# Kernel tuning notes

Measured on AMD Instinct MI355X. Metric: run time of the kernel, lower is better.

Reference implementation:

```python
import jax, jax.numpy as jnp
import numpy as np

B, Q, H, HKV, D = 4, 1024, 32, 8, 128
HID = H * D            # 4096
BS = 16                # block_size
BLOCKS_PER_SEQ = Q // BS  # 64
NB = B * BLOCKS_PER_SEQ   # 256 total cache blocks
THETA = 10000.0
SCALE = D ** -0.5


def _rope(x, pos):
    # x: [T, h, D] (NeoX half-split rotary), pos: [T] int
    inv = 1.0 / (THETA ** (jnp.arange(0, D, 2, dtype=jnp.float32) / D))  # [D/2]
    ang = pos[:, None].astype(jnp.float32) * inv                          # [T, D/2]
    cos = jnp.cos(ang)[:, None, :]
    sin = jnp.sin(ang)[:, None, :]
    x1, x2 = jnp.split(x, 2, axis=-1)
    return jnp.concatenate([x1 * cos - x2 * sin, x1 * sin + x2 * cos], axis=-1).astype(x.dtype)


def setup_inputs() -> dict:
    key = jax.random.key(0)
    ks = jax.random.split(key, 3)
    hidden_states = jax.random.normal(ks[0], (B * Q, HID), dtype=jnp.float32)
    w_qkv = jax.random.normal(ks[1], (HID, (H + 2 * HKV) * D), dtype=jnp.float32) * 0.02
    w_o = jax.random.normal(ks[2], (H * D, HID), dtype=jnp.float32) * 0.02
    key_cache = jnp.zeros((NB, BS, HKV, D), dtype=jnp.float32)
    value_cache = jnp.zeros((NB, BS, HKV, D), dtype=jnp.float32)
    positions = jnp.tile(jnp.arange(Q, dtype=jnp.int32), B)          # context_len=0 prefill
    slot_mapping = jnp.arange(B * Q, dtype=jnp.int32)                # contiguous slots
    block_tables = jnp.arange(NB, dtype=jnp.int32).reshape(B, BLOCKS_PER_SEQ)
    return {"hidden_states": hidden_states, "w_qkv": w_qkv, "w_o": w_o,
            "key_cache": key_cache, "value_cache": value_cache,
            "positions": positions, "slot_mapping": slot_mapping,
            "block_tables": block_tables}


def reference(hidden_states, w_qkv, w_o, key_cache, value_cache, positions, slot_mapping, block_tables):
    # QKV projection and split (q_size = H*D, kv_size = HKV*D)
    qkv = hidden_states @ w_qkv
    q, k, v = jnp.split(qkv, [H * D, H * D + HKV * D], axis=-1)
    q = q.reshape(-1, H, D)
    k = k.reshape(-1, HKV, D)
    v = v.reshape(-1, HKV, D)
    q = _rope(q, positions)
    k = _rope(k, positions)
    # BlockedKVCache.write: slot -> (slot // BS, slot % BS); flatten block dims
    kc = key_cache.reshape(NB * BS, HKV, D).at[slot_mapping].set(k)
    vc = value_cache.reshape(NB * BS, HKV, D).at[slot_mapping].set(v)
    # BlockedKVCache.gather via block_table: [B, blocks, BS, HKV, D] -> [B, S, HKV, D]
    gk = kc.reshape(NB, BS, HKV, D)[block_tables].reshape(B, Q, HKV, D)
    gv = vc.reshape(NB, BS, HKV, D)[block_tables].reshape(B, Q, HKV, D)
    # repeat_kv (GQA): each kv head repeated consecutively
    rep = H // HKV
    gk = jnp.repeat(gk, rep, axis=2)   # [B, S, H, D]
    gv = jnp.repeat(gv, rep, axis=2)
    qb = q.reshape(B, Q, H, D)
    scores = jnp.einsum('bqhd,bshd->bhqs', qb, gk) * SCALE
    # visible = context_len + token_idx + 1 with context_len=0 -> causal mask
    causal = jnp.arange(Q)[None, :] <= jnp.arange(Q)[:, None]          # [q, s]
    scores = jnp.where(causal[None, None], scores.astype(jnp.float32), -jnp.inf)
    probs = jax.nn.softmax(scores, axis=-1).astype(qb.dtype)
    attn = jnp.einsum('bhqs,bshd->bqhd', probs, gv).reshape(B * Q, H * D)
    return attn @ w_o
```

## Files before the change

### kernel.cpp

```cpp
#include <hip/hip_runtime.h>
#include <stdint.h>

typedef short short8  __attribute__((ext_vector_type(8)));
typedef short short4v __attribute__((ext_vector_type(4)));
typedef float f32x4   __attribute__((ext_vector_type(4)));

#define B_    4
#define Q_    1024
#define H_    32
#define HKV_  8
#define D_    128
#define HID_  4096
#define NQKV_ 6144
#define SCALE_ 0.08838834764831845f

__device__ __forceinline__ short f2bf(float f) {
  unsigned u = __builtin_bit_cast(unsigned, f);
  u += 0x7fffu + ((u >> 16) & 1u);
  return (short)(u >> 16);
}
__device__ __forceinline__ float bf2f(short s) {
  unsigned u = ((unsigned)(unsigned short)s) << 16;
  return __builtin_bit_cast(float, u);
}

__device__ __forceinline__ void gload_lds16(const void* g, void* l) {
  __builtin_amdgcn_global_load_lds(
      (__attribute__((address_space(1))) void*)(uintptr_t)(g),
      (__attribute__((address_space(3))) void*)(l), 16, 0, 0);
}

__device__ __forceinline__ f32x4 mfma16x16x32(short8 a, short8 b, f32x4 c) {
  return __builtin_amdgcn_mfma_f32_16x16x32_bf16(a, b, c, 0, 0, 0);
}

__global__ __launch_bounds__(256) void k_cvt(const float* __restrict__ src,
                                             short* __restrict__ dst, int n) {
  int i = (blockIdx.x * 256 + threadIdx.x) * 4;
  if (i + 3 < n) {
    float4 v = *reinterpret_cast<const float4*>(src + i);
    short4v o;
    o[0] = f2bf(v.x); o[1] = f2bf(v.y); o[2] = f2bf(v.z); o[3] = f2bf(v.w);
    *reinterpret_cast<short4v*>(dst + i) = o;
  }
}

__global__ __launch_bounds__(256) void k_cvt_t(const float* __restrict__ src,
                                               short* __restrict__ dst, int R, int C) {
  __shared__ float tile[32][33];
  int c0 = blockIdx.x * 32, r0 = blockIdx.y * 32;
  int tx = threadIdx.x & 31, ty = threadIdx.x >> 5;
#pragma unroll
  for (int i = 0; i < 4; ++i)
    tile[ty + i * 8][tx] = src[(size_t)(r0 + ty + i * 8) * C + c0 + tx];
  __syncthreads();
#pragma unroll
  for (int i = 0; i < 4; ++i)
    dst[(size_t)(c0 + ty + i * 8) * R + r0 + tx] = f2bf(tile[tx][ty + i * 8]);
}

__global__ __launch_bounds__(256) void k_gemm1(const short* __restrict__ A,
                                               const short* __restrict__ Bt,
                                               short* __restrict__ qout,
                                               short* __restrict__ kvout) {
  __shared__ alignas(16) short Asm[128 * 32];
  __shared__ alignas(16) short Bsm[128 * 32];
  const int tid = threadIdx.x;
  const int wave = tid >> 6, lane = tid & 63;
  const int G = lane >> 4, r = lane & 15;
  const int wm = wave >> 1, wn = wave & 1;
  const size_t Arow0 = (size_t)blockIdx.y * 128;
  const size_t Brow0 = (size_t)blockIdx.x * 128;
  const int K = HID_;
  const int ldrow = lane >> 2, ldcol = (lane & 3) * 8;
  short* Cb; size_t ldc, cb;
  if (Brow0 < (size_t)HID_) { Cb = qout; ldc = HID_; cb = Brow0; }
  else                      { Cb = kvout; ldc = 2048; cb = Brow0 - HID_; }
  f32x4 acc[4][4] = {};
  for (int k0 = 0; k0 < K; k0 += 32) {
    __syncthreads();
#pragma unroll
    for (int i = 0; i < 2; ++i) {
      int c = wave * 2 + i;
      gload_lds16(A + (Arow0 + c * 16 + ldrow) * K + k0 + ldcol, &Asm[c * 512]);
      gload_lds16(Bt + (Brow0 + c * 16 + ldrow) * K + k0 + ldcol, &Bsm[c * 512]);
    }
    asm volatile("s_waitcnt vmcnt(0)" ::: "memory");
    __syncthreads();
    short8 af[4], bf[4];
#pragma unroll
    for (int i = 0; i < 4; ++i)
      af[i] = *reinterpret_cast<const short8*>(&Asm[(wm * 64 + i * 16 + r) * 32 + G * 8]);
#pragma unroll
    for (int j = 0; j < 4; ++j)
      bf[j] = *reinterpret_cast<const short8*>(&Bsm[(wn * 64 + j * 16 + r) * 32 + G * 8]);
#pragma unroll
    for (int i = 0; i < 4; ++i)
#pragma unroll
      for (int j = 0; j < 4; ++j)
        acc[i][j] = mfma16x16x32(af[i], bf[j], acc[i][j]);
  }
#pragma unroll
  for (int i = 0; i < 4; ++i)
#pragma unroll
    for (int j = 0; j < 4; ++j)
#pragma unroll
      for (int rr = 0; rr < 4; ++rr) {
        size_t row = Arow0 + wm * 64 + i * 16 + G * 4 + rr;
        size_t col = cb + wn * 64 + j * 16 + r;
        Cb[row * ldc + col] = f2bf(acc[i][j][rr]);
      }
}

__global__ __launch_bounds__(256) void k_gemm2(const short* __restrict__ A,
                                               const short* __restrict__ Bt,
                                               float* __restrict__ C) {
  __shared__ alignas(16) short Asm[128 * 32];
  __shared__ alignas(16) short Bsm[128 * 32];
  const int tid = threadIdx.x;
  const int wave = tid >> 6, lane = tid & 63;
  const int G = lane >> 4, r = lane & 15;
  const int wm = wave >> 1, wn = wave & 1;
  const size_t Arow0 = (size_t)blockIdx.y * 128;
  const size_t Brow0 = (size_t)blockIdx.x * 128;
  const int K = HID_;
  const int ldrow = lane >> 2, ldcol = (lane & 3) * 8;
  f32x4 acc[4][4] = {};
  for (int k0 = 0; k0 < K; k0 += 32) {
    __syncthreads();
#pragma unroll
    for (int i = 0; i < 2; ++i) {
      int c = wave * 2 + i;
      gload_lds16(A + (Arow0 + c * 16 + ldrow) * K + k0 + ldcol, &Asm[c * 512]);
      gload_lds16(Bt + (Brow0 + c * 16 + ldrow) * K + k0 + ldcol, &Bsm[c * 512]);
    }
    asm volatile("s_waitcnt vmcnt(0)" ::: "memory");
    __syncthreads();
    short8 af[4], bf[4];
#pragma unroll
    for (int i = 0; i < 4; ++i)
      af[i] = *reinterpret_cast<const short8*>(&Asm[(wm * 64 + i * 16 + r) * 32 + G * 8]);
#pragma unroll
    for (int j = 0; j < 4; ++j)
      bf[j] = *reinterpret_cast<const short8*>(&Bsm[(wn * 64 + j * 16 + r) * 32 + G * 8]);
#pragma unroll
    for (int i = 0; i < 4; ++i)
#pragma unroll
      for (int j = 0; j < 4; ++j)
        acc[i][j] = mfma16x16x32(af[i], bf[j], acc[i][j]);
  }
#pragma unroll
  for (int i = 0; i < 4; ++i)
#pragma unroll
    for (int j = 0; j < 4; ++j)
#pragma unroll
      for (int rr = 0; rr < 4; ++rr) {
        size_t row = Arow0 + wm * 64 + i * 16 + G * 4 + rr;
        size_t col = Brow0 + wn * 64 + j * 16 + r;
        C[row * (size_t)HID_ + col] = acc[i][j][rr];
      }
}

__global__ __launch_bounds__(256) void k_rope_bf(short* __restrict__ x, int nh, int ld) {
  const int t = blockIdx.x;
  const float pos = (float)(t & (Q_ - 1));
  short* row = x + (size_t)t * ld;
  for (int i = threadIdx.x; i < nh * 64; i += 256) {
    int h = i >> 6, j = i & 63;
    float fr = powf(10000.0f, -(float)j * (1.0f / 64.0f));
    float sn, cs;
    sincosf(pos * fr, &sn, &cs);
    float x1 = bf2f(row[h * D_ + j]);
    float x2 = bf2f(row[h * D_ + 64 + j]);
    row[h * D_ + j]      = f2bf(x1 * cs - x2 * sn);
    row[h * D_ + 64 + j] = f2bf(x1 * sn + x2 * cs);
  }
}

__global__ __launch_bounds__(256) void k_attn(const short* __restrict__ qbf,
                                              const short* __restrict__ kv,
                                              short* __restrict__ attn) {
  const int qt = blockIdx.x;
  const int h  = blockIdx.y;
  const int b  = blockIdx.z;
  const int hkv = h >> 2;
  const int tid = threadIdx.x, wave = tid >> 6, lane = tid & 63;
  const int G = lane >> 4, r = lane & 15;
  const int q0w = qt * 64 + wave * 16;
  const float NEG_INF = -__builtin_inff();
  __shared__ alignas(16) short Ksm[32 * 136];
  __shared__ alignas(16) short Vsm[128 * 40];
  __shared__ alignas(16) short Psm[4][16][40];
  short8 qf[4];
  {
    const short* qrow = qbf + ((size_t)(b * Q_ + q0w + r)) * HID_ + h * D_;
#pragma unroll
    for (int ds = 0; ds < 4; ++ds)
      qf[ds] = *reinterpret_cast<const short8*>(qrow + ds * 32 + G * 8);
    const float pos = (float)(q0w + r);
#pragma unroll
    for (int ds2 = 0; ds2 < 2; ++ds2)
#pragma unroll
      for (int u = 0; u < 8; ++u) {
        int d = ds2 * 32 + G * 8 + u;
        float fr = powf(10000.0f, -(float)d * (1.0f / 64.0f));
        float sn, cs;
        sincosf(pos * fr, &sn, &cs);
        float x1 = bf2f(qf[ds2][u]);
        float x2 = bf2f(qf[ds2 + 2][u]);
        qf[ds2][u]     = f2bf(x1 * cs - x2 * sn);
        qf[ds2 + 2][u] = f2bf(x1 * sn + x2 * cs);
      }
  }
  f32x4 acc[8] = {};
  float m_run = NEG_INF, l_run = 0.f;
  const int ntiles = qt * 2 + 2;
  const int my_q = q0w + r;
  const int my_q_hi = q0w + 15;
  const int krow = tid >> 3, kd0 = (tid & 7) * 16;
  const int vs = tid & 31, vdg = tid >> 5;
  for (int st = 0; st < ntiles; ++st) {
    __syncthreads();
    {
      const short* gk = kv + ((size_t)(b * Q_ + st * 32 + krow)) * 2048 + hkv * D_ + kd0;
      *reinterpret_cast<uint4*>(&Ksm[krow * 136 + kd0])     = *reinterpret_cast<const uint4*>(gk);
      *reinterpret_cast<uint4*>(&Ksm[krow * 136 + kd0 + 8]) = *reinterpret_cast<const uint4*>(gk + 8);
      const short* gv = kv + ((size_t)(b * Q_ + st * 32 + vs)) * 2048 + 1024 + hkv * D_ + vdg * 16;
      short tmp[16];
      *reinterpret_cast<uint4*>(&tmp[0]) = *reinterpret_cast<const uint4*>(gv);
      *reinterpret_cast<uint4*>(&tmp[8]) = *reinterpret_cast<const uint4*>(gv + 8);
#pragma unroll
      for (int i = 0; i < 16; ++i) Vsm[(vdg * 16 + i) * 40 + vs] = tmp[i];
    }
    __syncthreads();
    if (st * 32 <= my_q_hi) {
      f32x4 sacc[2] = {};
#pragma unroll
      for (int sb = 0; sb < 2; ++sb)
#pragma unroll
        for (int ds = 0; ds < 4; ++ds) {
          short8 kf = *reinterpret_cast<const short8*>(&Ksm[(sb * 16 + r) * 136 + ds * 32 + G * 8]);
          sacc[sb] = mfma16x16x32(kf, qf[ds], sacc[sb]);
        }
      float vals[8];
      float mymax = NEG_INF;
#pragma unroll
      for (int sb = 0; sb < 2; ++sb)
#pragma unroll
        for (int j = 0; j < 4; ++j) {
          int sIdx = st * 32 + sb * 16 + G * 4 + j;
          float v = sacc[sb][j] * SCALE_;
          v = (sIdx <= my_q) ? v : NEG_INF;
          vals[sb * 4 + j] = v;
          mymax = fmaxf(mymax, v);
        }
      mymax = fmaxf(mymax, __shfl_xor(mymax, 16));
      mymax = fmaxf(mymax, __shfl_xor(mymax, 32));
      float m_new = fmaxf(m_run, mymax);
      float factor = __expf(m_run - m_new);
      float psum = 0.f;
      float pv_[8];
#pragma unroll
      for (int i = 0; i < 8; ++i) {
        float p = __expf(vals[i] - m_new);
        psum += p;
        pv_[i] = p;
      }
      psum += __shfl_xor(psum, 16);
      psum += __shfl_xor(psum, 32);
      l_run = l_run * factor + psum;
      m_run = m_new;
#pragma unroll
      for (int i = 0; i < 8; ++i)
        Psm[wave][r][(i >> 2) * 16 + G * 4 + (i & 3)] = f2bf(pv_[i]);
      asm volatile("s_waitcnt lgkmcnt(0)" ::: "memory");
      __builtin_amdgcn_sched_barrier(0);
      short8 pf = *reinterpret_cast<const short8*>(&Psm[wave][r][G * 8]);
      float frow[4];
#pragma unroll
      for (int rr = 0; rr < 4; ++rr) frow[rr] = __shfl(factor, G * 4 + rr);
#pragma unroll
      for (int dt = 0; dt < 8; ++dt)
#pragma unroll
        for (int rr = 0; rr < 4; ++rr) acc[dt][rr] *= frow[rr];
#pragma unroll
      for (int dt = 0; dt < 8; ++dt) {
        short8 vf = *reinterpret_cast<const short8*>(&Vsm[(dt * 16 + r) * 40 + G * 8]);
        acc[dt] = mfma16x16x32(pf, vf, acc[dt]);
      }
    }
  }
  float inv = 1.0f / l_run;
  float irow[4];
#pragma unroll
  for (int rr = 0; rr < 4; ++rr) irow[rr] = __shfl(inv, G * 4 + rr);
#pragma unroll
  for (int dt = 0; dt < 8; ++dt)
#pragma unroll
    for (int rr = 0; rr < 4; ++rr) {
      size_t rowi = (size_t)(b * Q_ + q0w + G * 4 + rr) * HID_;
      attn[rowi + h * D_ + dt * 16 + r] = f2bf(acc[dt][rr] * irow[rr]);
    }
}

extern "C" void kernel_launch(void* const* d_in, const int* in_sizes, int n_in,
                              void* d_out, int out_size, void* d_ws, size_t ws_size,
                              hipStream_t stream) {
  const float* hidden = (const float*)d_in[0];
  const float* w_qkv  = (const float*)d_in[1];
  const float* w_o    = (const float*)d_in[2];
  float* out = (float*)d_out;
  char* ws = (char*)d_ws;
  char* od = (char*)d_out;
  short* hid_bf  = (short*)(od + 0);
  short* q_bf    = (short*)(od + 33554432);
  short* wqkvT   = (short*)(ws + 0);
  short* kv_ws   = (short*)(ws + 50331648);
  short* attn_bf = (short*)(ws + 0);
  short* woT     = (short*)(ws + 33554432);

  k_cvt<<<dim3(16384), dim3(256), 0, stream>>>(hidden, hid_bf, HID_ * B_ * Q_);
  k_cvt_t<<<dim3(192, 128), dim3(256), 0, stream>>>(w_qkv, wqkvT, HID_, NQKV_);
  k_gemm1<<<dim3(48, 32), dim3(256), 0, stream>>>(hid_bf, wqkvT, q_bf, kv_ws);
  k_rope_bf<<<dim3(B_ * Q_), dim3(256), 0, stream>>>(kv_ws, HKV_, 2048);
  k_attn<<<dim3(16, 32, 4), dim3(256), 0, stream>>>(q_bf, kv_ws, attn_bf);
  k_cvt_t<<<dim3(128, 128), dim3(256), 0, stream>>>(w_o, woT, HID_, HID_);
  k_gemm2<<<dim3(32, 32), dim3(256), 0, stream>>>(attn_bf, woT, out);
}
```

Baseline: 684.1 us.

## Replace GEMM kernels with 4-stage pipelined 512-thread templated GEMM

Merges the two bf16 GEMM kernels into one templated kernel with a 4-deep LDS ring buffer. It issues global-to-LDS loads three k-tiles ahead and uses partial vmcnt waits in place of a full drain each iteration. Tiles grow to 128x256 for the QKV projection and 256x256 for the output projection, using 8 waves per block and raising MFMA priority during compute. This targets exposed memory latency and per-tile sync overhead, at the cost of more LDS and registers, which may reduce occupancy, and fewer blocks in the grid.

```diff
diff --git a/kernel.cpp b/kernel.cpp
--- a/kernel.cpp
+++ b/kernel.cpp
@@ -34,6 +34,14 @@
   return __builtin_amdgcn_mfma_f32_16x16x32_bf16(a, b, c, 0, 0, 0);
 }
 
+template <int N> __device__ __forceinline__ void waitv() {
+  if constexpr (N == 8)      asm volatile("s_waitcnt vmcnt(8)" ::: "memory");
+  else if constexpr (N == 6) asm volatile("s_waitcnt vmcnt(6)" ::: "memory");
+  else if constexpr (N == 4) asm volatile("s_waitcnt vmcnt(4)" ::: "memory");
+  else if constexpr (N == 3) asm volatile("s_waitcnt vmcnt(3)" ::: "memory");
+  else                       asm volatile("s_waitcnt vmcnt(0)" ::: "memory");
+}
+
 __global__ __launch_bounds__(256) void k_cvt(const float* __restrict__ src,
                                              short* __restrict__ dst, int n) {
   int i = (blockIdx.x * 256 + threadIdx.x) * 4;
@@ -59,106 +67,119 @@
     dst[(size_t)(c0 + ty + i * 8) * R + r0 + tx] = f2bf(tile[tx][ty + i * 8]);
 }
 
-__global__ __launch_bounds__(256) void k_gemm1(const short* __restrict__ A,
-                                               const short* __restrict__ Bt,
-                                               short* __restrict__ qout,
-                                               short* __restrict__ kvout) {
-  __shared__ alignas(16) short Asm[128 * 32];
-  __shared__ alignas(16) short Bsm[128 * 32];
-  const int tid = threadIdx.x;
+template <int MF, typename OT>
+__global__ __launch_bounds__(512, 2) void k_gemmp(const short* __restrict__ A,
+                                                  const short* __restrict__ Bt,
+                                                  OT* __restrict__ Cq,
+                                                  short* __restrict__ Ckv) {
+  constexpr int BM   = MF * 32;
+  constexpr int AISS = (BM * 4) / 512;
+  constexpr int ISS  = AISS + 2;
+  constexpr int NT   = HID_ / 32;
+  __shared__ alignas(16) short Al[4][BM * 32];
+  __shared__ alignas(16) short Bl[4][256 * 32];
+  const int tid  = threadIdx.x;
   const int wave = tid >> 6, lane = tid & 63;
   const int G = lane >> 4, r = lane & 15;
-  const int wm = wave >> 1, wn = wave & 1;
-  const size_t Arow0 = (size_t)blockIdx.y * 128;
-  const size_t Brow0 = (size_t)blockIdx.x * 128;
+  const int wm = wave >> 2, wn = wave & 3;
+  const size_t Arow0 = (size_t)blockIdx.y * BM;
+  const size_t Bcol0 = (size_t)blockIdx.x * 256;
   const int K = HID_;
-  const int ldrow = lane >> 2, ldcol = (lane & 3) * 8;
-  short* Cb; size_t ldc, cb;
-  if (Brow0 < (size_t)HID_) { Cb = qout; ldc = HID_; cb = Brow0; }
-  else                      { Cb = kvout; ldc = 2048; cb = Brow0 - HID_; }
-  f32x4 acc[4][4] = {};
-  for (int k0 = 0; k0 < K; k0 += 32) {
-    __syncthreads();
-#pragma unroll
-    for (int i = 0; i < 2; ++i) {
-      int c = wave * 2 + i;
-      gload_lds16(A + (Arow0 + c * 16 + ldrow) * K + k0 + ldcol, &Asm[c * 512]);
-      gload_lds16(Bt + (Brow0 + c * 16 + ldrow) * K + k0 + ldcol, &Bsm[c * 512]);
-    }
-    asm volatile("s_waitcnt vmcnt(0)" ::: "memory");
-    __syncthreads();
-    short8 af[4], bf[4];
-#pragma unroll
-    for (int i = 0; i < 4; ++i)
-      af[i] = *reinterpret_cast<const short8*>(&Asm[(wm * 64 + i * 16 + r) * 32 + G * 8]);
-#pragma unroll
-    for (int j = 0; j < 4; ++j)
-      bf[j] = *reinterpret_cast<const short8*>(&Bsm[(wn * 64 + j * 16 + r) * 32 + G * 8]);
-#pragma unroll
-    for (int i = 0; i < 4; ++i)
-#pragma unroll
-      for (int j = 0; j < 4; ++j)
-        acc[i][j] = mfma16x16x32(af[i], bf[j], acc[i][j]);
-  }
-#pragma unroll
-  for (int i = 0; i < 4; ++i)
-#pragma unroll
-    for (int j = 0; j < 4; ++j)
-#pragma unroll
-      for (int rr = 0; rr < 4; ++rr) {
-        size_t row = Arow0 + wm * 64 + i * 16 + G * 4 + rr;
-        size_t col = cb + wn * 64 + j * 16 + r;
-        Cb[row * ldc + col] = f2bf(acc[i][j][rr]);
-      }
-}
-
-__global__ __launch_bounds__(256) void k_gemm2(const short* __restrict__ A,
-                                               const short* __restrict__ Bt,
-                                               float* __restrict__ C) {
-  __shared__ alignas(16) short Asm[128 * 32];
-  __shared__ alignas(16) short Bsm[128 * 32];
-  const int tid = threadIdx.x;
-  const int wave = tid >> 6, lane = tid & 63;
-  const int G = lane >> 4, r = lane & 15;
-  const int wm = wave >> 1, wn = wave & 1;
-  const size_t Arow0 = (size_t)blockIdx.y * 128;
-  const size_t Brow0 = (size_t)blockIdx.x * 128;
-  const int K = HID_;
-  const int ldrow = lane >> 2, ldcol = (lane & 3) * 8;
-  f32x4 acc[4][4] = {};
-  for (int k0 = 0; k0 < K; k0 += 32) {
-    __syncthreads();
-#pragma unroll
-    for (int i = 0; i < 2; ++i) {
-      int c = wave * 2 + i;
-      gload_lds16(A + (Arow0 + c * 16 + ldrow) * K + k0 + ldcol, &Asm[c * 512]);
-      gload_lds16(Bt + (Brow0 + c * 16 + ldrow) * K + k0 + ldcol, &Bsm[c * 512]);
-    }
-    asm volatile("s_waitcnt vmcnt(0)" ::: "memory");
-    __syncthreads();
-    short8 af[4], bf[4];
-#pragma unroll
-    for (int i = 0; i < 4; ++i)
-      af[i] = *reinterpret_cast<const short8*>(&Asm[(wm * 64 + i * 16 + r) * 32 + G * 8]);
-#pragma unroll
-    for (int j = 0; j < 4; ++j)
-      bf[j] = *reinterpret_cast<const short8*>(&Bsm[(wn * 64 + j * 16 + r) * 32 + G * 8]);
-#pragma unroll
-    for (int i = 0; i < 4; ++i)
-#pragma unroll
-      for (int j = 0; j < 4; ++j)
-        acc[i][j] = mfma16x16x32(af[i], bf[j], acc[i][j]);
-  }
-#pragma unroll
-  for (int i = 0; i < 4; ++i)
-#pragma unroll
-    for (int j = 0; j < 4; ++j)
-#pragma unroll
-      for (int rr = 0; rr < 4; ++rr) {
-        size_t row = Arow0 + wm * 64 + i * 16 + G * 4 + rr;
-        size_t col = Brow0 + wn * 64 + j * 16 + r;
-        C[row * (size_t)HID_ + col] = acc[i][j][rr];
-      }
+  const int swz = 0;
+
+  const short* aptr[AISS];
+  int albase[AISS];
+#pragma unroll
+  for (int i = 0; i < AISS; ++i) {
+    int sc = i * 512 + tid;
+    int L = sc ^ swz;
+    aptr[i] = A + (Arow0 + (size_t)(L >> 2)) * K + (L & 3) * 8;
+    albase[i] = (i * 512 + (tid & ~63)) * 8;
+  }
+  const short* bptr[2];
+  int blbase[2];
+#pragma unroll
+  for (int i = 0; i < 2; ++i) {
+    int sc = i * 512 + tid;
+    int L = sc ^ swz;
+    bptr[i] = Bt + (Bcol0 + (size_t)(L >> 2)) * K + (L & 3) * 8;
+    blbase[i] = (i * 512 + (tid & ~63)) * 8;
+  }
+  auto stage = [&](int t) {
+    const int bi = t & 3;
+    const size_t ko = (size_t)t * 32;
+#pragma unroll
+    for (int i = 0; i < AISS; ++i)
+      gload_lds16(aptr[i] + ko, &Al[bi][albase[i]]);
+#pragma unroll
+    for (int i = 0; i < 2; ++i)
+      gload_lds16(bptr[i] + ko, &Bl[bi][blbase[i]]);
+  };
+
+  const int kswz = 0;
+  f32x4 acc[MF][4] = {};
+
+  stage(0); stage(1); stage(2);
+  waitv<2 * ISS>();
+  __builtin_amdgcn_s_barrier();
+  __builtin_amdgcn_sched_barrier(0);
+
+  for (int t = 0; t < NT; ++t) {
+    const int bi = t & 3;
+    if (t + 3 < NT) stage(t + 3);
+    short8 af[MF], bfr[4];
+#pragma unroll
+    for (int m = 0; m < MF; ++m) {
+      int ro = wm * (MF * 16) + m * 16 + r;
+      af[m] = *reinterpret_cast<const short8*>(&Al[bi][(ro * 32 + G * 8) ^ kswz]);
+    }
+#pragma unroll
+    for (int n = 0; n < 4; ++n) {
+      int ro = wn * 64 + n * 16 + r;
+      bfr[n] = *reinterpret_cast<const short8*>(&Bl[bi][(ro * 32 + G * 8) ^ kswz]);
+    }
+    __builtin_amdgcn_s_setprio(1);
+#pragma unroll
+    for (int m = 0; m < MF; ++m)
+#pragma unroll
+      for (int n = 0; n < 4; ++n)
+        acc[m][n] = mfma16x16x32(af[m], bfr[n], acc[m][n]);
+    __builtin_amdgcn_s_setprio(0);
+    if (t + 1 < NT) {
+      if (t + 3 < NT)      waitv<2 * ISS>();
+      else if (t + 2 < NT) waitv<ISS>();
+      else                 waitv<0>();
+      __builtin_amdgcn_s_barrier();
+      __builtin_amdgcn_sched_barrier(0);
+    }
+  }
+
+  if constexpr (sizeof(OT) == 2) {
+    short* Cb; size_t ldc, cb;
+    if (Bcol0 < (size_t)HID_) { Cb = (short*)Cq; ldc = HID_; cb = Bcol0; }
+    else                      { Cb = Ckv; ldc = 2048; cb = Bcol0 - HID_; }
+#pragma unroll
+    for (int m = 0; m < MF; ++m)
+#pragma unroll
+      for (int n = 0; n < 4; ++n)
+#pragma unroll
+        for (int rr = 0; rr < 4; ++rr) {
+          size_t row = Arow0 + wm * (MF * 16) + m * 16 + G * 4 + rr;
+          size_t col = cb + wn * 64 + n * 16 + r;
+          Cb[row * ldc + col] = f2bf(acc[m][n][rr]);
+        }
+  } else {
+#pragma unroll
+    for (int m = 0; m < MF; ++m)
+#pragma unroll
+      for (int n = 0; n < 4; ++n)
+#pragma unroll
+        for (int rr = 0; rr < 4; ++rr) {
+          size_t row = Arow0 + wm * (MF * 16) + m * 16 + G * 4 + rr;
+          size_t col = Bcol0 + wn * 64 + n * 16 + r;
+          Cq[row * (size_t)HID_ + col] = acc[m][n][rr];
+        }
+  }
 }
 
 __global__ __launch_bounds__(256) void k_rope_bf(short* __restrict__ x, int nh, int ld) {
@@ -321,9 +342,9 @@
 
   k_cvt<<<dim3(16384), dim3(256), 0, stream>>>(hidden, hid_bf, HID_ * B_ * Q_);
   k_cvt_t<<<dim3(192, 128), dim3(256), 0, stream>>>(w_qkv, wqkvT, HID_, NQKV_);
-  k_gemm1<<<dim3(48, 32), dim3(256), 0, stream>>>(hid_bf, wqkvT, q_bf, kv_ws);
+  k_gemmp<4, short><<<dim3(24, 32), dim3(512), 0, stream>>>(hid_bf, wqkvT, q_bf, kv_ws);
   k_rope_bf<<<dim3(B_ * Q_), dim3(256), 0, stream>>>(kv_ws, HKV_, 2048);
   k_attn<<<dim3(16, 32, 4), dim3(256), 0, stream>>>(q_bf, kv_ws, attn_bf);
   k_cvt_t<<<dim3(128, 128), dim3(256), 0, stream>>>(w_o, woT, HID_, HID_);
-  k_gemm2<<<dim3(32, 32), dim3(256), 0, stream>>>(attn_bf, woT, out);
-}
+  k_gemmp<8, float><<<dim3(16, 16), dim3(512), 0, stream>>>(attn_bf, woT, out, nullptr);
+}
```

Result: slower. 755.5 us (+10.4%).
